# Optimization experiments

Hardware: AMD Instinct MI355X
Metric: run time of the kernel (lower is better)

## Reference

```python
import jax, jax.numpy as jnp
import numpy as np

B, EMBED, STATE, HIDDEN, HORIZON = 16384, 512, 128, 256, 32


def setup_inputs() -> dict:
    key = jax.random.key(0)
    ks = jax.random.split(key, 14)
    s = 0.05
    return {
        "embedding": jax.random.normal(ks[0], (B, EMBED), jnp.float32),
        "initial_state": jax.random.normal(ks[1], (B, STATE), jnp.float32),
        # input projection: embed_dim -> hidden_dim
        "Wp": jax.random.normal(ks[2], (HIDDEN, EMBED), jnp.float32) * s,
        "bp": jnp.zeros((HIDDEN,), jnp.float32),
        # GRU layer 0 (input = state_dim), gate order r,z,n as in PyTorch
        "Wih0": jax.random.normal(ks[3], (3 * HIDDEN, STATE), jnp.float32) * s,
        "Whh0": jax.random.normal(ks[4], (3 * HIDDEN, HIDDEN), jnp.float32) * s,
        "bih0": jax.random.normal(ks[5], (3 * HIDDEN,), jnp.float32) * s,
        "bhh0": jax.random.normal(ks[6], (3 * HIDDEN,), jnp.float32) * s,
        # GRU layer 1 (input = hidden_dim)
        "Wih1": jax.random.normal(ks[7], (3 * HIDDEN, HIDDEN), jnp.float32) * s,
        "Whh1": jax.random.normal(ks[8], (3 * HIDDEN, HIDDEN), jnp.float32) * s,
        "bih1": jax.random.normal(ks[9], (3 * HIDDEN,), jnp.float32) * s,
        "bhh1": jax.random.normal(ks[10], (3 * HIDDEN,), jnp.float32) * s,
        # output projection: hidden_dim -> state_dim
        "Wo": jax.random.normal(ks[11], (STATE, HIDDEN), jnp.float32) * s,
        "bo": jnp.zeros((STATE,), jnp.float32),
    }


def _gru_cell(x, h, Wih, Whh, bih, bhh):
    # PyTorch GRU cell: gates ordered (r, z, n)
    gi = x @ Wih.T + bih            # [B, 3H]
    gh = h @ Whh.T + bhh            # [B, 3H]
    ir, iz, inn = jnp.split(gi, 3, axis=-1)
    hr, hz, hn = jnp.split(gh, 3, axis=-1)
    r = jax.nn.sigmoid(ir + hr)
    z = jax.nn.sigmoid(iz + hz)
    n = jnp.tanh(inn + r * hn)
    return (1.0 - z) * n + z * h


def reference(embedding, initial_state, Wp, bp, Wih0, Whh0, bih0, bhh0,
              Wih1, Whh1, bih1, bhh1, Wo, bo):
    # Initial hidden for both GRU layers = projected embedding (repeated)
    h_init = embedding @ Wp.T + bp  # [B, H]

    def step(carry, _):
        h0, h1, state = carry
        h0 = _gru_cell(state, h0, Wih0, Whh0, bih0, bhh0)
        h1 = _gru_cell(h0, h1, Wih1, Whh1, bih1, bhh1)
        next_state = h1 @ Wo.T + bo  # [B, state_dim]
        return (h0, h1, next_state), next_state

    _, states = jax.lax.scan(step, (h_init, h_init, initial_state), None,
                             length=HORIZON)
    return jnp.transpose(states, (1, 0, 2))  # [B, horizon, state_dim]
```

## Files before the change

kernel.cpp:

```cpp
#include <hip/hip_runtime.h>


#define BTOT    16384
#define EMBED   512
#define STATE   128
#define HIDDEN  256
#define HORIZON 32

#define ROWS_PER_BLK 32
#define MT           (ROWS_PER_BLK / 16)
#define THREADS      512

typedef __attribute__((ext_vector_type(4))) float f32x4;
typedef __attribute__((ext_vector_type(8))) short s16x8;

#define N_Wp    (HIDDEN*EMBED)
#define N_Wih0  (3*HIDDEN*STATE)
#define N_Whh0  (3*HIDDEN*HIDDEN)
#define N_Wih1  (3*HIDDEN*HIDDEN)
#define N_Whh1  (3*HIDDEN*HIDDEN)
#define N_Wo    (STATE*HIDDEN)
#define OFF_Wp   0
#define OFF_Wih0 (OFF_Wp   + N_Wp)
#define OFF_Whh0 (OFF_Wih0 + N_Wih0)
#define OFF_Wih1 (OFF_Whh0 + N_Whh0)
#define OFF_Whh1 (OFF_Wih1 + N_Wih1)
#define OFF_Wo   (OFF_Whh1 + N_Whh1)
#define N_WTOT   (OFF_Wo   + N_Wo)

__device__ __forceinline__ short f2bf(float f) {
    unsigned u = __float_as_uint(f);
    u += 0x7FFFu + ((u >> 16) & 1u);
    return (short)(u >> 16);
}
__device__ __forceinline__ float bf2f(short h) {
    return __uint_as_float(((unsigned)(unsigned short)h) << 16);
}
__device__ __forceinline__ void split8(const f32x4 a, const f32x4 b, s16x8 &hi, s16x8 &lo) {
#pragma unroll
    for (int i = 0; i < 4; i++) {
        short h = f2bf(a[i]); hi[i] = h; lo[i] = f2bf(a[i] - bf2f(h));
    }
#pragma unroll
    for (int i = 0; i < 4; i++) {
        short h = f2bf(b[i]); hi[4+i] = h; lo[4+i] = f2bf(b[i] - bf2f(h));
    }
}

__device__ __forceinline__ int sidx(int row, int col) {
    return row * 256 + ((((col >> 3) ^ (row & 7)) << 3) | (col & 7));
}
__device__ __forceinline__ int sfrag(int row, int k0) {
    return row * 256 + (((k0 >> 3) ^ (row & 7)) << 3);
}

__device__ __forceinline__ int fswz(int row, int col) {
    return row * EMBED + ((((col >> 2) ^ (row & 7)) << 2) | (col & 3));
}
__device__ __forceinline__ void lds_frag_f32(const float* H, int row, int k0,
                                             s16x8 &hi, s16x8 &lo) {
    int base = row * EMBED;
    int s0 = (((k0 >> 2)    ) ^ (row & 7)) << 2;
    int s1 = (((k0 >> 2) + 1) ^ (row & 7)) << 2;
    f32x4 a = *(const f32x4*)(H + base + s0);
    f32x4 b = *(const f32x4*)(H + base + s1);
    split8(a, b, hi, lo);
}

#define MFMA(A, B, C) __builtin_amdgcn_mfma_f32_16x16x32_bf16(A, B, C, 0, 0, 0)

template<int KW>
__device__ __forceinline__ void catblock(f32x4 (&acc)[MT],
                                         const s16x8 (&ahi)[MT], const s16x8 (&alo)[MT],
                                         const short* __restrict__ WHi,
                                         const short* __restrict__ WLo,
                                         int wr, int k0) {
    s16x8 bhi = *(const s16x8*)(WHi + wr * KW + k0);
    s16x8 blo = *(const s16x8*)(WLo + wr * KW + k0);
#pragma unroll
    for (int mt = 0; mt < MT; mt++) acc[mt] = MFMA(ahi[mt], bhi, acc[mt]);
#pragma unroll
    for (int mt = 0; mt < MT; mt++) acc[mt] = MFMA(alo[mt], bhi, acc[mt]);
#pragma unroll
    for (int mt = 0; mt < MT; mt++) acc[mt] = MFMA(ahi[mt], blo, acc[mt]);
}

__device__ __forceinline__ float sigf(float x)  { return 1.0f / (1.0f + __expf(-x)); }
__device__ __forceinline__ float tanhf_(float x){ return 1.0f - 2.0f / (__expf(2.0f * x) + 1.0f); }

template<int KI, bool AGLOB>
__device__ __forceinline__ void gru_layer(
    const short* __restrict__ AiHi, const short* __restrict__ AiLo,
    const short* __restrict__ HHi,  const short* __restrict__ HLo,
    const short* __restrict__ WihHi, const short* __restrict__ WihLo,
    const short* __restrict__ WhhHi, const short* __restrict__ WhhLo,
    const float br[2], const float bz[2], const float bi[2], const float bh[2],
    int rowbase, int wave, int lr, int lg,
    float hnew[2][MT][4])
{
#pragma unroll
    for (int p = 0; p < 2; p++) {
        f32x4 aR[MT], aZ[MT], aI[MT], aH[MT];
        {
            f32x4 zz = {0.f, 0.f, 0.f, 0.f};
#pragma unroll
            for (int mt = 0; mt < MT; mt++) { aR[mt]=zz; aZ[mt]=zz; aI[mt]=zz; aH[mt]=zz; }
        }
        const int hcol = wave * 32 + p * 16 + lr;
#pragma unroll 2
        for (int kc = 0; kc < KI / 32; kc++) {
            const int k0 = kc * 32 + lg * 8;
            s16x8 ahi[MT], alo[MT];
#pragma unroll
            for (int mt = 0; mt < MT; mt++) {
                if constexpr (AGLOB) {
                    size_t base = (size_t)(rowbase + mt * 16 + lr) * KI + k0;
                    ahi[mt] = *(const s16x8*)(AiHi + base);
                    alo[mt] = *(const s16x8*)(AiLo + base);
                } else {
                    int off = sfrag(mt * 16 + lr, k0);
                    ahi[mt] = *(const s16x8*)(AiHi + off);
                    alo[mt] = *(const s16x8*)(AiLo + off);
                }
            }
            catblock<KI>(aR, ahi, alo, WihHi, WihLo, 0 * HIDDEN + hcol, k0);
            catblock<KI>(aZ, ahi, alo, WihHi, WihLo, 1 * HIDDEN + hcol, k0);
            catblock<KI>(aI, ahi, alo, WihHi, WihLo, 2 * HIDDEN + hcol, k0);
        }
#pragma unroll 2
        for (int kc = 0; kc < HIDDEN / 32; kc++) {
            const int k0 = kc * 32 + lg * 8;
            s16x8 ahi[MT], alo[MT];
#pragma unroll
            for (int mt = 0; mt < MT; mt++) {
                int off = sfrag(mt * 16 + lr, k0);
                ahi[mt] = *(const s16x8*)(HHi + off);
                alo[mt] = *(const s16x8*)(HLo + off);
            }
            catblock<HIDDEN>(aR, ahi, alo, WhhHi, WhhLo, 0 * HIDDEN + hcol, k0);
            catblock<HIDDEN>(aZ, ahi, alo, WhhHi, WhhLo, 1 * HIDDEN + hcol, k0);
            catblock<HIDDEN>(aH, ahi, alo, WhhHi, WhhLo, 2 * HIDDEN + hcol, k0);
        }
#pragma unroll
        for (int mt = 0; mt < MT; mt++)
#pragma unroll
            for (int j = 0; j < 4; j++) {
                int row  = mt * 16 + lg * 4 + j;
                float r  = sigf(aR[mt][j] + br[p]);
                float z  = sigf(aZ[mt][j] + bz[p]);
                float n  = tanhf_(aI[mt][j] + bi[p] + r * (aH[mt][j] + bh[p]));
                float ho = bf2f(HHi[sidx(row, hcol)]) + bf2f(HLo[sidx(row, hcol)]);
                hnew[p][mt][j] = (1.0f - z) * n + z * ho;
            }
    }
}

__device__ __forceinline__ void write_h(short* HHi, short* HLo, const float hnew[2][MT][4],
                                        int wave, int lr, int lg) {
#pragma unroll
    for (int p = 0; p < 2; p++) {
        int col = wave * 32 + p * 16 + lr;
#pragma unroll
        for (int mt = 0; mt < MT; mt++)
#pragma unroll
            for (int j = 0; j < 4; j++) {
                int row = mt * 16 + lg * 4 + j;
                float v = hnew[p][mt][j];
                short hi = f2bf(v);
                short lo = f2bf(v - bf2f(hi));
                HHi[sidx(row, col)] = hi;
                HLo[sidx(row, col)] = lo;
            }
    }
}

__global__ void prep_split(const float* __restrict__ Wp,   const float* __restrict__ Wih0,
                           const float* __restrict__ Whh0, const float* __restrict__ Wih1,
                           const float* __restrict__ Whh1, const float* __restrict__ Wo,
                           short* __restrict__ hi, short* __restrict__ lo) {
    int i = blockIdx.x * 256 + threadIdx.x;
    if (i >= N_WTOT) return;
    float w;
    if      (i < OFF_Wih0) w = Wp  [i - OFF_Wp];
    else if (i < OFF_Whh0) w = Wih0[i - OFF_Wih0];
    else if (i < OFF_Wih1) w = Whh0[i - OFF_Whh0];
    else if (i < OFF_Whh1) w = Wih1[i - OFF_Wih1];
    else if (i < OFF_Wo)   w = Whh1[i - OFF_Whh1];
    else                   w = Wo  [i - OFF_Wo];
    short h = f2bf(w);
    hi[i] = h;
    lo[i] = f2bf(w - bf2f(h));
}

__global__ void prep_state(const float* __restrict__ s0,
                           short* __restrict__ shi, short* __restrict__ slo) {
    int i = blockIdx.x * 256 + threadIdx.x;
    if (i >= BTOT * STATE) return;
    float w = s0[i];
    short h = f2bf(w);
    shi[i] = h;
    slo[i] = f2bf(w - bf2f(h));
}

__global__ __launch_bounds__(THREADS, 4)
void gru_main(const float* __restrict__ emb,
              const float* __restrict__ bp,
              const float* __restrict__ bih0, const float* __restrict__ bhh0,
              const float* __restrict__ bih1, const float* __restrict__ bhh1,
              const float* __restrict__ bo,
              const short* __restrict__ Whi,  const short* __restrict__ Wlo,
              short* __restrict__ Shi, short* __restrict__ Slo,
              float* __restrict__ out) {
    __shared__ short sH[4 * ROWS_PER_BLK * HIDDEN];
    short* H0hi = sH;
    short* H0lo = sH + 1 * ROWS_PER_BLK * HIDDEN;
    short* H1hi = sH + 2 * ROWS_PER_BLK * HIDDEN;
    short* H1lo = sH + 3 * ROWS_PER_BLK * HIDDEN;
    float* fl   = (float*)sH;

    const int tid  = threadIdx.x;
    const int wave = tid >> 6, lane = tid & 63;
    const int lr = lane & 15, lg = lane >> 4;
    const int rowbase = blockIdx.x * ROWS_PER_BLK;

    const short *WpHi   = Whi + OFF_Wp,   *WpLo   = Wlo + OFF_Wp;
    const short *Wih0Hi = Whi + OFF_Wih0, *Wih0Lo = Wlo + OFF_Wih0;
    const short *Whh0Hi = Whi + OFF_Whh0, *Whh0Lo = Wlo + OFF_Whh0;
    const short *Wih1Hi = Whi + OFF_Wih1, *Wih1Lo = Wlo + OFF_Wih1;
    const short *Whh1Hi = Whi + OFF_Whh1, *Whh1Lo = Wlo + OFF_Whh1;
    const short *WoHi   = Whi + OFF_Wo,   *WoLo   = Wlo + OFF_Wo;

    float br0[2], bz0[2], bi0[2], bh0[2];
    float br1[2], bz1[2], bi1[2], bh1[2];
#pragma unroll
    for (int p = 0; p < 2; p++) {
        int c = wave * 32 + p * 16 + lr;
        br0[p] = bih0[c] + bhh0[c];
        bz0[p] = bih0[HIDDEN + c] + bhh0[HIDDEN + c];
        bi0[p] = bih0[2 * HIDDEN + c];
        bh0[p] = bhh0[2 * HIDDEN + c];
        br1[p] = bih1[c] + bhh1[c];
        bz1[p] = bih1[HIDDEN + c] + bhh1[HIDDEN + c];
        bi1[p] = bih1[2 * HIDDEN + c];
        bh1[p] = bhh1[2 * HIDDEN + c];
    }
    const int scol = wave * 16 + lr;
    const float bo_v = bo[scol];
    float bpv[2];
    bpv[0] = bp[wave * 32 + lr];
    bpv[1] = bp[wave * 32 + 16 + lr];

    for (int idx = tid; idx < ROWS_PER_BLK * EMBED; idx += THREADS) {
        int r = idx >> 9, c = idx & (EMBED - 1);
        fl[fswz(r, c)] = emb[(size_t)(rowbase + r) * EMBED + c];
    }
    __syncthreads();
    f32x4 hacc[2][MT];
    {
        f32x4 zz = {0.f, 0.f, 0.f, 0.f};
#pragma unroll
        for (int nt = 0; nt < 2; nt++)
#pragma unroll
            for (int mt = 0; mt < MT; mt++) hacc[nt][mt] = zz;
    }
#pragma unroll 2
    for (int kc = 0; kc < EMBED / 32; kc++) {
        const int k0 = kc * 32 + lg * 8;
        s16x8 ahi[MT], alo[MT];
#pragma unroll
        for (int mt = 0; mt < MT; mt++)
            lds_frag_f32(fl, mt * 16 + lr, k0, ahi[mt], alo[mt]);
#pragma unroll
        for (int nt = 0; nt < 2; nt++)
            catblock<EMBED>(hacc[nt], ahi, alo, WpHi, WpLo, wave * 32 + nt * 16 + lr, k0);
    }
    __syncthreads();
#pragma unroll
    for (int nt = 0; nt < 2; nt++)
#pragma unroll
        for (int mt = 0; mt < MT; mt++)
#pragma unroll
            for (int j = 0; j < 4; j++) {
                int row = mt * 16 + lg * 4 + j;
                int col = wave * 32 + nt * 16 + lr;
                float v = hacc[nt][mt][j] + bpv[nt];
                short hi = f2bf(v);
                short lo = f2bf(v - bf2f(hi));
                H0hi[sidx(row, col)] = hi;  H0lo[sidx(row, col)] = lo;
                H1hi[sidx(row, col)] = hi;  H1lo[sidx(row, col)] = lo;
            }
    __syncthreads();

#pragma unroll 1
    for (int t = 0; t < HORIZON; t++) {
        float hn0[2][MT][4];
        gru_layer<STATE, true>(Shi, Slo, H0hi, H0lo,
                               Wih0Hi, Wih0Lo, Whh0Hi, Whh0Lo,
                               br0, bz0, bi0, bh0,
                               rowbase, wave, lr, lg, hn0);
        __syncthreads();
        write_h(H0hi, H0lo, hn0, wave, lr, lg);
        __syncthreads();

        float hn1[2][MT][4];
        gru_layer<HIDDEN, false>(H0hi, H0lo, H1hi, H1lo,
                                 Wih1Hi, Wih1Lo, Whh1Hi, Whh1Lo,
                                 br1, bz1, bi1, bh1,
                                 rowbase, wave, lr, lg, hn1);
        __syncthreads();
        write_h(H1hi, H1lo, hn1, wave, lr, lg);
        __syncthreads();

        f32x4 o[MT];
        {
            f32x4 zz = {0.f, 0.f, 0.f, 0.f};
#pragma unroll
            for (int mt = 0; mt < MT; mt++) o[mt] = zz;
        }
#pragma unroll 2
        for (int kc = 0; kc < HIDDEN / 32; kc++) {
            const int k0 = kc * 32 + lg * 8;
            s16x8 ahi[MT], alo[MT];
#pragma unroll
            for (int mt = 0; mt < MT; mt++) {
                int off = sfrag(mt * 16 + lr, k0);
                ahi[mt] = *(const s16x8*)(H1hi + off);
                alo[mt] = *(const s16x8*)(H1lo + off);
            }
            catblock<HIDDEN>(o, ahi, alo, WoHi, WoLo, scol, k0);
        }
#pragma unroll
        for (int mt = 0; mt < MT; mt++)
#pragma unroll
            for (int j = 0; j < 4; j++) {
                int row   = mt * 16 + lg * 4 + j;
                size_t gr = (size_t)(rowbase + row);
                float v   = o[mt][j] + bo_v;
                out[gr * (size_t)(HORIZON * STATE) + (size_t)t * STATE + scol] = v;
                short hi = f2bf(v);
                short lo = f2bf(v - bf2f(hi));
                Shi[gr * STATE + scol] = hi;
                Slo[gr * STATE + scol] = lo;
            }
        __threadfence_block();
        __syncthreads();
    }
}

extern "C" void kernel_launch(void* const* d_in, const int* in_sizes, int n_in,
                              void* d_out, int out_size, void* d_ws, size_t ws_size,
                              hipStream_t stream) {
    (void)in_sizes; (void)n_in; (void)out_size; (void)ws_size;
    const float* emb  = (const float*)d_in[0];
    const float* st0  = (const float*)d_in[1];
    const float* Wp   = (const float*)d_in[2];
    const float* bp   = (const float*)d_in[3];
    const float* Wih0 = (const float*)d_in[4];
    const float* Whh0 = (const float*)d_in[5];
    const float* bih0 = (const float*)d_in[6];
    const float* bhh0 = (const float*)d_in[7];
    const float* Wih1 = (const float*)d_in[8];
    const float* Whh1 = (const float*)d_in[9];
    const float* bih1 = (const float*)d_in[10];
    const float* bhh1 = (const float*)d_in[11];
    const float* Wo   = (const float*)d_in[12];
    const float* bo   = (const float*)d_in[13];
    float* out = (float*)d_out;

    short* shi = (short*)d_ws;
    short* slo = shi + (size_t)BTOT * STATE;
    short* whi = slo + (size_t)BTOT * STATE;
    short* wlo = whi + N_WTOT;

    prep_split<<<(N_WTOT + 255) / 256, 256, 0, stream>>>(Wp, Wih0, Whh0, Wih1, Whh1, Wo, whi, wlo);
    prep_state<<<(BTOT * STATE + 255) / 256, 256, 0, stream>>>(st0, shi, slo);
    gru_main<<<BTOT / ROWS_PER_BLK, THREADS, 0, stream>>>(
        emb, bp, bih0, bhh0, bih1, bhh1, bo, whi, wlo, shi, slo, out);
}
```

Before: 6.600 ms.

## Double rows per block and prepack weights into lane-contiguous MFMA fragments

Each block now handles 64 rows instead of 32, so every weight fragment fetched from global memory is reused across twice as many MFMA tiles. Weights are prepacked so each wave lane reads one contiguous 16-byte fragment per chunk, giving fully coalesced loads. The r/z/n gate MFMAs are interleaved and the k-loops fully unrolled to expose more independent work. In exchange, register and LDS pressure rise (launch bounds drop to 2 blocks per CU) and there are half as many blocks.

```diff
diff --git a/kernel.cpp b/kernel.cpp
--- a/kernel.cpp
+++ b/kernel.cpp
@@ -7,26 +7,21 @@
 #define HIDDEN  256
 #define HORIZON 32
 
-#define ROWS_PER_BLK 32
-#define MT           (ROWS_PER_BLK / 16)
+#define ROWS_PER_BLK 64
+#define MT           4
 #define THREADS      512
 
 typedef __attribute__((ext_vector_type(4))) float f32x4;
 typedef __attribute__((ext_vector_type(8))) short s16x8;
 
-#define N_Wp    (HIDDEN*EMBED)
-#define N_Wih0  (3*HIDDEN*STATE)
-#define N_Whh0  (3*HIDDEN*HIDDEN)
-#define N_Wih1  (3*HIDDEN*HIDDEN)
-#define N_Whh1  (3*HIDDEN*HIDDEN)
-#define N_Wo    (STATE*HIDDEN)
-#define OFF_Wp   0
-#define OFF_Wih0 (OFF_Wp   + N_Wp)
-#define OFF_Whh0 (OFF_Wih0 + N_Wih0)
-#define OFF_Wih1 (OFF_Whh0 + N_Whh0)
-#define OFF_Whh1 (OFF_Wih1 + N_Wih1)
-#define OFF_Wo   (OFF_Whh1 + N_Whh1)
-#define N_WTOT   (OFF_Wo   + N_Wo)
+#define N_WTOT   851968
+#define CH_Wp    0
+#define CH_Wih0  256
+#define CH_Whh0  448
+#define CH_Wih1  832
+#define CH_Whh1  1216
+#define CH_Wo    1600
+#define N_CHUNK  1664
 
 __device__ __forceinline__ short f2bf(float f) {
     unsigned u = __float_as_uint(f);
@@ -69,20 +64,46 @@
 
 #define MFMA(A, B, C) __builtin_amdgcn_mfma_f32_16x16x32_bf16(A, B, C, 0, 0, 0)
 
-template<int KW>
-__device__ __forceinline__ void catblock(f32x4 (&acc)[MT],
-                                         const s16x8 (&ahi)[MT], const s16x8 (&alo)[MT],
-                                         const short* __restrict__ WHi,
-                                         const short* __restrict__ WLo,
-                                         int wr, int k0) {
-    s16x8 bhi = *(const s16x8*)(WHi + wr * KW + k0);
-    s16x8 blo = *(const s16x8*)(WLo + wr * KW + k0);
-#pragma unroll
-    for (int mt = 0; mt < MT; mt++) acc[mt] = MFMA(ahi[mt], bhi, acc[mt]);
-#pragma unroll
-    for (int mt = 0; mt < MT; mt++) acc[mt] = MFMA(alo[mt], bhi, acc[mt]);
-#pragma unroll
-    for (int mt = 0; mt < MT; mt++) acc[mt] = MFMA(ahi[mt], blo, acc[mt]);
+__device__ __forceinline__ void catrow(f32x4 (&aC0)[MT], f32x4 (&aC1)[MT], f32x4 (&aC2)[MT],
+                                       const s16x8 (&ahi)[MT], const s16x8 (&alo)[MT],
+                                       const s16x8* __restrict__ Vh,
+                                       const s16x8* __restrict__ Vl,
+                                       int c0, int c1, int c2, int lane) {
+    s16x8 bh0 = Vh[c0 * 64 + lane], bl0 = Vl[c0 * 64 + lane];
+    s16x8 bh1 = Vh[c1 * 64 + lane], bl1 = Vl[c1 * 64 + lane];
+    s16x8 bh2 = Vh[c2 * 64 + lane], bl2 = Vl[c2 * 64 + lane];
+#pragma unroll
+    for (int mt = 0; mt < MT; mt++) aC0[mt] = MFMA(ahi[mt], bh0, aC0[mt]);
+#pragma unroll
+    for (int mt = 0; mt < MT; mt++) aC1[mt] = MFMA(ahi[mt], bh1, aC1[mt]);
+#pragma unroll
+    for (int mt = 0; mt < MT; mt++) aC2[mt] = MFMA(ahi[mt], bh2, aC2[mt]);
+#pragma unroll
+    for (int mt = 0; mt < MT; mt++) aC0[mt] = MFMA(alo[mt], bh0, aC0[mt]);
+#pragma unroll
+    for (int mt = 0; mt < MT; mt++) aC1[mt] = MFMA(alo[mt], bh1, aC1[mt]);
+#pragma unroll
+    for (int mt = 0; mt < MT; mt++) aC2[mt] = MFMA(alo[mt], bh2, aC2[mt]);
+#pragma unroll
+    for (int mt = 0; mt < MT; mt++) aC0[mt] = MFMA(ahi[mt], bl0, aC0[mt]);
+#pragma unroll
+    for (int mt = 0; mt < MT; mt++) aC1[mt] = MFMA(ahi[mt], bl1, aC1[mt]);
+#pragma unroll
+    for (int mt = 0; mt < MT; mt++) aC2[mt] = MFMA(ahi[mt], bl2, aC2[mt]);
+}
+
+__device__ __forceinline__ void catone(f32x4 (&acc)[MT],
+                                       const s16x8 (&ahi)[MT], const s16x8 (&alo)[MT],
+                                       const s16x8* __restrict__ Vh,
+                                       const s16x8* __restrict__ Vl,
+                                       int c, int lane) {
+    s16x8 bh = Vh[c * 64 + lane], bl = Vl[c * 64 + lane];
+#pragma unroll
+    for (int mt = 0; mt < MT; mt++) acc[mt] = MFMA(ahi[mt], bh, acc[mt]);
+#pragma unroll
+    for (int mt = 0; mt < MT; mt++) acc[mt] = MFMA(alo[mt], bh, acc[mt]);
+#pragma unroll
+    for (int mt = 0; mt < MT; mt++) acc[mt] = MFMA(ahi[mt], bl, acc[mt]);
 }
 
 __device__ __forceinline__ float sigf(float x)  { return 1.0f / (1.0f + __expf(-x)); }
@@ -92,12 +113,13 @@
 __device__ __forceinline__ void gru_layer(
     const short* __restrict__ AiHi, const short* __restrict__ AiLo,
     const short* __restrict__ HHi,  const short* __restrict__ HLo,
-    const short* __restrict__ WihHi, const short* __restrict__ WihLo,
-    const short* __restrict__ WhhHi, const short* __restrict__ WhhLo,
+    const s16x8* __restrict__ Vh,   const s16x8* __restrict__ Vl,
+    int ihBase, int hhBase,
     const float br[2], const float bz[2], const float bi[2], const float bh[2],
-    int rowbase, int wave, int lr, int lg,
+    int rowbase, int wave, int lane, int lr, int lg,
     float hnew[2][MT][4])
 {
+    constexpr int NKC_I = KI / 32;
 #pragma unroll
     for (int p = 0; p < 2; p++) {
         f32x4 aR[MT], aZ[MT], aI[MT], aH[MT];
@@ -106,9 +128,10 @@
 #pragma unroll
             for (int mt = 0; mt < MT; mt++) { aR[mt]=zz; aZ[mt]=zz; aI[mt]=zz; aH[mt]=zz; }
         }
-        const int hcol = wave * 32 + p * 16 + lr;
-#pragma unroll 2
-        for (int kc = 0; kc < KI / 32; kc++) {
+        const int gb = wave * 2 + p;
+        const int hcol = gb * 16 + lr;
+#pragma unroll
+        for (int kc = 0; kc < NKC_I; kc++) {
             const int k0 = kc * 32 + lg * 8;
             s16x8 ahi[MT], alo[MT];
 #pragma unroll
@@ -123,12 +146,13 @@
                     alo[mt] = *(const s16x8*)(AiLo + off);
                 }
             }
-            catblock<KI>(aR, ahi, alo, WihHi, WihLo, 0 * HIDDEN + hcol, k0);
-            catblock<KI>(aZ, ahi, alo, WihHi, WihLo, 1 * HIDDEN + hcol, k0);
-            catblock<KI>(aI, ahi, alo, WihHi, WihLo, 2 * HIDDEN + hcol, k0);
+            catrow(aR, aZ, aI, ahi, alo, Vh, Vl,
+                   ihBase + (gb     ) * NKC_I + kc,
+                   ihBase + (gb + 16) * NKC_I + kc,
+                   ihBase + (gb + 32) * NKC_I + kc, lane);
         }
-#pragma unroll 2
-        for (int kc = 0; kc < HIDDEN / 32; kc++) {
+#pragma unroll
+        for (int kc = 0; kc < 8; kc++) {
             const int k0 = kc * 32 + lg * 8;
             s16x8 ahi[MT], alo[MT];
 #pragma unroll
@@ -137,9 +161,10 @@
                 ahi[mt] = *(const s16x8*)(HHi + off);
                 alo[mt] = *(const s16x8*)(HLo + off);
             }
-            catblock<HIDDEN>(aR, ahi, alo, WhhHi, WhhLo, 0 * HIDDEN + hcol, k0);
-            catblock<HIDDEN>(aZ, ahi, alo, WhhHi, WhhLo, 1 * HIDDEN + hcol, k0);
-            catblock<HIDDEN>(aH, ahi, alo, WhhHi, WhhLo, 2 * HIDDEN + hcol, k0);
+            catrow(aR, aZ, aH, ahi, alo, Vh, Vl,
+                   hhBase + (gb     ) * 8 + kc,
+                   hhBase + (gb + 16) * 8 + kc,
+                   hhBase + (gb + 32) * 8 + kc, lane);
         }
 #pragma unroll
         for (int mt = 0; mt < MT; mt++)
@@ -174,19 +199,27 @@
     }
 }
 
-__global__ void prep_split(const float* __restrict__ Wp,   const float* __restrict__ Wih0,
-                           const float* __restrict__ Whh0, const float* __restrict__ Wih1,
-                           const float* __restrict__ Whh1, const float* __restrict__ Wo,
-                           short* __restrict__ hi, short* __restrict__ lo) {
+__global__ void prep_pack(const float* __restrict__ Wp,   const float* __restrict__ Wih0,
+                          const float* __restrict__ Whh0, const float* __restrict__ Wih1,
+                          const float* __restrict__ Whh1, const float* __restrict__ Wo,
+                          short* __restrict__ hi, short* __restrict__ lo) {
     int i = blockIdx.x * 256 + threadIdx.x;
     if (i >= N_WTOT) return;
-    float w;
-    if      (i < OFF_Wih0) w = Wp  [i - OFF_Wp];
-    else if (i < OFF_Whh0) w = Wih0[i - OFF_Wih0];
-    else if (i < OFF_Wih1) w = Whh0[i - OFF_Whh0];
-    else if (i < OFF_Whh1) w = Wih1[i - OFF_Wih1];
-    else if (i < OFF_Wo)   w = Whh1[i - OFF_Whh1];
-    else                   w = Wo  [i - OFF_Wo];
+    int chunk = i >> 9;
+    int s     = i & 511;
+    int lane  = s >> 3, j = s & 7;
+    int lr = lane & 15, lg = lane >> 4;
+    const float* src; int c, NKC, K;
+    if      (chunk < CH_Wih0) { src = Wp;   c = chunk;           NKC = 16; K = 512; }
+    else if (chunk < CH_Whh0) { src = Wih0; c = chunk - CH_Wih0; NKC = 4;  K = 128; }
+    else if (chunk < CH_Wih1) { src = Whh0; c = chunk - CH_Whh0; NKC = 8;  K = 256; }
+    else if (chunk < CH_Whh1) { src = Wih1; c = chunk - CH_Wih1; NKC = 8;  K = 256; }
+    else if (chunk < CH_Wo)   { src = Whh1; c = chunk - CH_Whh1; NKC = 8;  K = 256; }
+    else                      { src = Wo;   c = chunk - CH_Wo;   NKC = 8;  K = 256; }
+    int g  = c / NKC, kc = c % NKC;
+    int row = g * 16 + lr;
+    int col = kc * 32 + lg * 8 + j;
+    float w = src[(size_t)row * K + col];
     short h = f2bf(w);
     hi[i] = h;
     lo[i] = f2bf(w - bf2f(h));
@@ -202,7 +235,7 @@
     slo[i] = f2bf(w - bf2f(h));
 }
 
-__global__ __launch_bounds__(THREADS, 4)
+__global__ __launch_bounds__(THREADS, 2)
 void gru_main(const float* __restrict__ emb,
               const float* __restrict__ bp,
               const float* __restrict__ bih0, const float* __restrict__ bhh0,
@@ -223,12 +256,8 @@
     const int lr = lane & 15, lg = lane >> 4;
     const int rowbase = blockIdx.x * ROWS_PER_BLK;
 
-    const short *WpHi   = Whi + OFF_Wp,   *WpLo   = Wlo + OFF_Wp;
-    const short *Wih0Hi = Whi + OFF_Wih0, *Wih0Lo = Wlo + OFF_Wih0;
-    const short *Whh0Hi = Whi + OFF_Whh0, *Whh0Lo = Wlo + OFF_Whh0;
-    const short *Wih1Hi = Whi + OFF_Wih1, *Wih1Lo = Wlo + OFF_Wih1;
-    const short *Whh1Hi = Whi + OFF_Whh1, *Whh1Lo = Wlo + OFF_Whh1;
-    const short *WoHi   = Whi + OFF_Wo,   *WoLo   = Wlo + OFF_Wo;
+    const s16x8* Vh = (const s16x8*)Whi;
+    const s16x8* Vl = (const s16x8*)Wlo;
 
     float br0[2], bz0[2], bi0[2], bh0[2];
     float br1[2], bz1[2], bi1[2], bh1[2];
@@ -272,7 +301,7 @@
             lds_frag_f32(fl, mt * 16 + lr, k0, ahi[mt], alo[mt]);
 #pragma unroll
         for (int nt = 0; nt < 2; nt++)
-            catblock<EMBED>(hacc[nt], ahi, alo, WpHi, WpLo, wave * 32 + nt * 16 + lr, k0);
+            catone(hacc[nt], ahi, alo, Vh, Vl, CH_Wp + (wave * 2 + nt) * 16 + kc, lane);
     }
     __syncthreads();
 #pragma unroll
@@ -294,19 +323,19 @@
 #pragma unroll 1
     for (int t = 0; t < HORIZON; t++) {
         float hn0[2][MT][4];
-        gru_layer<STATE, true>(Shi, Slo, H0hi, H0lo,
-                               Wih0Hi, Wih0Lo, Whh0Hi, Whh0Lo,
+        gru_layer<STATE, true>(Shi, Slo, H0hi, H0lo, Vh, Vl,
+                               CH_Wih0, CH_Whh0,
                                br0, bz0, bi0, bh0,
-                               rowbase, wave, lr, lg, hn0);
+                               rowbase, wave, lane, lr, lg, hn0);
         __syncthreads();
         write_h(H0hi, H0lo, hn0, wave, lr, lg);
         __syncthreads();
 
         float hn1[2][MT][4];
-        gru_layer<HIDDEN, false>(H0hi, H0lo, H1hi, H1lo,
-                                 Wih1Hi, Wih1Lo, Whh1Hi, Whh1Lo,
+        gru_layer<HIDDEN, false>(H0hi, H0lo, H1hi, H1lo, Vh, Vl,
+                                 CH_Wih1, CH_Whh1,
                                  br1, bz1, bi1, bh1,
-                                 rowbase, wave, lr, lg, hn1);
+                                 rowbase, wave, lane, lr, lg, hn1);
         __syncthreads();
         write_h(H1hi, H1lo, hn1, wave, lr, lg);
         __syncthreads();
@@ -317,8 +346,8 @@
 #pragma unroll
             for (int mt = 0; mt < MT; mt++) o[mt] = zz;
         }
-#pragma unroll 2
-        for (int kc = 0; kc < HIDDEN / 32; kc++) {
+#pragma unroll
+        for (int kc = 0; kc < 8; kc++) {
             const int k0 = kc * 32 + lg * 8;
             s16x8 ahi[MT], alo[MT];
 #pragma unroll
@@ -327,7 +356,7 @@
                 ahi[mt] = *(const s16x8*)(H1hi + off);
                 alo[mt] = *(const s16x8*)(H1lo + off);
             }
-            catblock<HIDDEN>(o, ahi, alo, WoHi, WoLo, scol, k0);
+            catone(o, ahi, alo, Vh, Vl, CH_Wo + wave * 8 + kc, lane);
         }
 #pragma unroll
         for (int mt = 0; mt < MT; mt++)
@@ -372,7 +401,7 @@
     short* whi = slo + (size_t)BTOT * STATE;
     short* wlo = whi + N_WTOT;
 
-    prep_split<<<(N_WTOT + 255) / 256, 256, 0, stream>>>(Wp, Wih0, Whh0, Wih1, Whh1, Wo, whi, wlo);
+    prep_pack<<<(N_WTOT + 255) / 256, 256, 0, stream>>>(Wp, Wih0, Whh0, Wih1, Whh1, Wo, whi, wlo);
     prep_state<<<(BTOT * STATE + 255) / 256, 256, 0, stream>>>(st0, shi, slo);
     gru_main<<<BTOT / ROWS_PER_BLK, THREADS, 0, stream>>>(
         emb, bp, bih0, bhh0, bih1, bhh1, bo, whi, wlo, shi, slo, out);
```

Result: slower. 7.973 ms (+20.8%).
